# Optimization experiments

Hardware: AMD Instinct MI355X
Metric: run time of the kernel (lower is better)

Reference implementation:

```python
import jax
import jax.numpy as jnp
import numpy as np

NB_FEATURES = 512
DIM_EXPLOSION_FACTOR = 20
MB_DIM = NB_FEATURES * DIM_EXPLOSION_FACTOR  # 10240
NB_PROJ_ENTRIES = 6   # nonzeros per row of the random projection
HASH_LENGTH = 32      # k for k-winner-take-all
NB_CLASSES = 100
BATCH = 8192


def _make_rand_proj(key):
    # Sparse binary projection: each MB neuron samples NB_PROJ_ENTRIES inputs.
    r = jax.random.uniform(key, (MB_DIM, NB_FEATURES), dtype=jnp.float32)
    th = jax.lax.top_k(r, NB_PROJ_ENTRIES)[0][:, -1:]  # per-row k-th largest
    return (r >= th).astype(jnp.float32)  # [MB_DIM, NB_FEATURES], ~6 ones/row


def setup_inputs() -> dict:
    key = jax.random.key(0)
    k1, k2, k3, k4 = jax.random.split(key, 4)
    x = jax.random.normal(k1, (BATCH, NB_FEATURES), dtype=jnp.float32)
    w1 = _make_rand_proj(k2)
    # PositiveLinear params (kaiming-uniform-ish scale)
    bound = 1.0 / np.sqrt(MB_DIM)
    w2 = jax.random.uniform(k3, (NB_CLASSES, MB_DIM), dtype=jnp.float32,
                            minval=-bound, maxval=bound)
    b2 = jax.random.uniform(k4, (NB_CLASSES,), dtype=jnp.float32,
                            minval=-bound, maxval=bound)
    return {"x": x, "w1": w1, "w2": w2, "b2": b2}


def reference(x, w1, w2, b2):
    # MB projection: dense matmul with the (non-learned) random projection.
    h = jnp.einsum("bf,mf->bm", x, w1)  # [B, MB_DIM]
    # k-winner-take-all sparsify: keep the HASH_LENGTH largest values per row.
    th = jax.lax.top_k(h, HASH_LENGTH)[0][:, -1:]  # k-th largest per row
    h = jnp.where(h >= th, h, jnp.zeros((), h.dtype))
    # PositiveLinear: weights clamped to min=0 before the linear.
    w2c = jnp.maximum(w2, 0.0)
    return jnp.einsum("bm,cm->bc", h, w2c) + b2  # [B, NB_CLASSES]
```

## Files before the change

kernel.cpp:

```cpp
#include <hip/hip_runtime.h>
#include <stdint.h>

typedef unsigned int uint;
typedef unsigned short ushort;

#define NB_FEATURES 512
#define MB_DIM      10240
#define NB_CLASSES  100
#define BATCH       8192
#define KSEL        32
#define NTHR        256
#define VPT         40
#define MAXOVF      512

static __device__ __forceinline__ uint f2key(float f) {
    uint u = __float_as_uint(f);
    return u ^ (0x80000000u | (uint)((int)u >> 31));
}
static __device__ __forceinline__ float key2f(uint k) {
    uint u = k ^ (0x80000000u | (uint)(((int)~k) >> 31));
    return __uint_as_float(u);
}

__global__ __launch_bounds__(256) void k_extract(const float* __restrict__ w1,
                                                 uint2* __restrict__ idx2,
                                                 uint* __restrict__ ovfc,
                                                 uint2* __restrict__ ovfe) {
    __shared__ ushort scr[4][8];
    const int gw   = (blockIdx.x * 256 + threadIdx.x) >> 6;
    const int lane = threadIdx.x & 63;
    const int wid  = (threadIdx.x >> 6) & 3;

    const float* row = w1 + (size_t)gw * NB_FEATURES;
    const float4 a = *(const float4*)(row + lane * 8);
    const float4 b = *(const float4*)(row + lane * 8 + 4);
    const float v[8] = {a.x, a.y, a.z, a.w, b.x, b.y, b.z, b.w};
    int cnt = 0;
#pragma unroll
    for (int j = 0; j < 8; ++j) cnt += (v[j] > 0.5f);
    int p = cnt;
#pragma unroll
    for (int off = 1; off < 64; off <<= 1) {
        int n = __shfl_up(p, off, 64);
        if (lane >= off) p += n;
    }
    const int total = __shfl(p, 63, 64);
    int slot = p - cnt;

    if (lane < 8) scr[wid][lane] = (ushort)NB_FEATURES;
    __syncthreads();
#pragma unroll
    for (int j = 0; j < 8; ++j) {
        if (v[j] > 0.5f) {
            if (slot < 8) scr[wid][slot] = (ushort)(lane * 8 + j);
            slot++;
        }
    }
    __syncthreads();
    if (lane == 0) {
        const uint c0 = scr[wid][0], c1 = scr[wid][1], c2 = scr[wid][2];
        const uint c3 = scr[wid][3], c4 = scr[wid][4], c5 = scr[wid][5];
        const uint c6 = scr[wid][6], c7 = scr[wid][7];
        uint2 q;
        q.x = c0 | (c1 << 10) | (c2 << 20);
        q.y = c3 | (c4 << 10) | (c5 << 20);
        idx2[gw] = q;
        if (total > 6) {
            const uint s = atomicAdd(ovfc, 1u);
            if (s < MAXOVF) {
                uint2 e; e.x = (uint)gw; e.y = c6 | (c7 << 10);
                ovfe[s] = e;
            }
        }
    }
}

__global__ __launch_bounds__(256) void k_w2t(const float* __restrict__ w2,
                                             float* __restrict__ w2t) {
    const int i = blockIdx.x * 256 + threadIdx.x;
    if (i >= NB_CLASSES * MB_DIM) return;
    const int c = i / MB_DIM;
    const int m = i - c * MB_DIM;
    w2t[(size_t)m * NB_CLASSES + c] = fmaxf(w2[i], 0.0f);
}

template <bool USE_W2T>
__global__ __launch_bounds__(NTHR) void k_main(
    const float* __restrict__ x, const uint2* __restrict__ idx2,
    const uint* __restrict__ ovfc, const uint2* __restrict__ ovfe,
    const float* __restrict__ w2t, const float* __restrict__ w2,
    const float* __restrict__ b2, float* __restrict__ out)
{
    __shared__ float xs4[513 * 4];
    __shared__ float cand[512];
    __shared__ uint  s_wsum[4];
    __shared__ float s_piv[4];
    __shared__ float s_thf;
    __shared__ uint  s_cnt1;
    __shared__ uint  s_pref;
    __shared__ int   s_k;
    __shared__ uint  list_m[64];
    __shared__ float list_v[64];

    const int tid  = threadIdx.x;
    const int lane = tid & 63;
    const int wid  = tid >> 6;
    const int brow = blockIdx.x;

    {
        const float v0 = x[(size_t)brow * NB_FEATURES + tid];
        const float v1 = x[(size_t)brow * NB_FEATURES + tid + 256];
        float4 f0; f0.x = v0; f0.y = v0; f0.z = v0; f0.w = v0;
        float4 f1; f1.x = v1; f1.y = v1; f1.z = v1; f1.w = v1;
        *(float4*)&xs4[tid << 2]         = f0;
        *(float4*)&xs4[(tid + 256) << 2] = f1;
        if (tid == 0) {
            float4 z; z.x = 0.0f; z.y = 0.0f; z.z = 0.0f; z.w = 0.0f;
            *(float4*)&xs4[512 << 2] = z;
        }
        if (tid < 64) { list_m[tid] = 0u; list_v[tid] = 0.0f; }
    }
    __syncthreads();

    const float* xb = xs4 + (tid & 3);

    float vals[VPT];
#pragma unroll
    for (int i = 0; i < VPT; ++i) {
        const int m = tid + (i << 8);
        const uint2 q = idx2[m];
        float s = xb[(q.x & 1023u) << 2];
        s += xb[((q.x >> 10) & 1023u) << 2];
        s += xb[((q.x >> 20) & 1023u) << 2];
        s += xb[(q.y & 1023u) << 2];
        s += xb[((q.y >> 10) & 1023u) << 2];
        s += xb[((q.y >> 20) & 1023u) << 2];
        vals[i] = s;
    }

    {
        uint novf = *ovfc;
        if (novf > MAXOVF) novf = MAXOVF;
        for (uint e = 0; e < novf; ++e) {
            const uint2 ent = ovfe[e];
            const float add = xb[(ent.y & 1023u) << 2]
                            + xb[((ent.y >> 10) & 1023u) << 2];
            const int em = (int)ent.x;
#pragma unroll
            for (int i = 0; i < VPT; ++i) {
                if (em == tid + (i << 8)) vals[i] += add;
            }
        }
    }

    {
        float v = vals[0];
#pragma unroll
        for (int i = 1; i < VPT; ++i) v = fmaxf(v, vals[i]);
#pragma unroll
        for (int k = 2; k <= 64; k <<= 1) {
#pragma unroll
            for (int j = k >> 1; j > 0; j >>= 1) {
                const float pr = __shfl_xor(v, j, 64);
                const bool lower = (lane & j) == 0;
                const bool asc   = (lane & k) == 0;
                const float mn = fminf(v, pr), mx = fmaxf(v, pr);
                v = (lower == asc) ? mx : mn;
            }
        }
        if (lane == 31) s_piv[wid] = v;
    }
    __syncthreads();
    float pivot = fmaxf(fmaxf(s_piv[0], s_piv[1]), fmaxf(s_piv[2], s_piv[3]));

    int myc = 0;
#pragma unroll
    for (int i = 0; i < VPT; ++i) myc += (vals[i] >= pivot) ? 1 : 0;
    int p = myc;
#pragma unroll
    for (int off = 1; off < 64; off <<= 1) {
        int n = __shfl_up(p, off, 64);
        if (lane >= off) p += n;
    }
    if (lane == 63) s_wsum[wid] = (uint)p;
    __syncthreads();
    int base = p - myc;
    for (int w = 0; w < wid; ++w) base += (int)s_wsum[w];
    const int ctot = (int)(s_wsum[0] + s_wsum[1] + s_wsum[2] + s_wsum[3]);
    {
        int slot = base;
#pragma unroll
        for (int i = 0; i < VPT; ++i) {
            if (vals[i] >= pivot) {
                if (slot < 512) cand[slot] = vals[i];
                slot++;
            }
        }
    }
    __syncthreads();

    if (ctot <= 512) {
        for (int pos = tid; pos < ctot; pos += NTHR) {
            const float u = cand[pos];
            int rank = 0;
            for (int j = 0; j < ctot; ++j) {
                const float vv = cand[j];
                rank += ((vv > u) || (vv == u && j < pos)) ? 1 : 0;
            }
            if (rank == KSEL - 1) s_thf = u;
        }
    } else {
        if (tid == 0) { s_pref = 0u; s_k = KSEL; }
        __syncthreads();
        for (int bit = 31; bit >= 0; --bit) {
            const uint bmask = 1u << bit;
            const uint dmask = (bit == 31) ? 0u : (0xFFFFFFFFu << (bit + 1));
            const uint pref = s_pref;
            int mc = 0;
#pragma unroll
            for (int i = 0; i < VPT; ++i) {
                const uint k = f2key(vals[i]);
                mc += (((k & dmask) == pref) && (k & bmask)) ? 1 : 0;
            }
            if (tid == 0) s_cnt1 = 0;
            __syncthreads();
            if (mc) atomicAdd(&s_cnt1, (uint)mc);
            __syncthreads();
            if (tid == 0) {
                if ((int)s_cnt1 >= s_k) s_pref = pref | bmask;
                else s_k -= (int)s_cnt1;
            }
            __syncthreads();
        }
        if (tid == 0) s_thf = key2f(s_pref);
    }
    __syncthreads();
    const float thf = s_thf;

    int kc = 0;
#pragma unroll
    for (int i = 0; i < VPT; ++i) kc += (vals[i] >= thf) ? 1 : 0;
    int p2 = kc;
#pragma unroll
    for (int off = 1; off < 64; off <<= 1) {
        int n = __shfl_up(p2, off, 64);
        if (lane >= off) p2 += n;
    }
    if (lane == 63) s_wsum[wid] = (uint)p2;
    __syncthreads();
    int kbase = p2 - kc;
    for (int w = 0; w < wid; ++w) kbase += (int)s_wsum[w];
    {
        int slot = kbase;
#pragma unroll
        for (int i = 0; i < VPT; ++i) {
            if (vals[i] >= thf) {
                if (slot < 64) {
                    list_m[slot] = (uint)(tid + (i << 8));
                    list_v[slot] = vals[i];
                }
                slot++;
            }
        }
    }
    __syncthreads();

    if (tid < NB_CLASSES) {
        float a0 = b2[tid], a1 = 0.0f;
#pragma unroll
        for (int j = 0; j < 64; j += 2) {
            const uint m0 = list_m[j], m1 = list_m[j + 1];
            float w0, w1;
            if (USE_W2T) {
                w0 = w2t[(size_t)m0 * NB_CLASSES + tid];
                w1 = w2t[(size_t)m1 * NB_CLASSES + tid];
            } else {
                w0 = fmaxf(w2[(size_t)tid * MB_DIM + m0], 0.0f);
                w1 = fmaxf(w2[(size_t)tid * MB_DIM + m1], 0.0f);
            }
            a0 = fmaf(list_v[j],     w0, a0);
            a1 = fmaf(list_v[j + 1], w1, a1);
        }
        out[(size_t)brow * NB_CLASSES + tid] = a0 + a1;
    }
}

extern "C" void kernel_launch(void* const* d_in, const int* in_sizes, int n_in,
                              void* d_out, int out_size, void* d_ws, size_t ws_size,
                              hipStream_t stream) {
    const float* x  = (const float*)d_in[0];
    const float* w1 = (const float*)d_in[1];
    const float* w2 = (const float*)d_in[2];
    const float* b2 = (const float*)d_in[3];
    float* out = (float*)d_out;

    uint2* idx2 = (uint2*)d_ws;
    uint*  ovfc = (uint*)((char*)d_ws + 81920);
    uint2* ovfe = (uint2*)((char*)d_ws + 81928);
    const size_t W2T_OFF = 131072;
    float* w2t = (float*)((char*)d_ws + W2T_OFF);
    const bool use_w2t =
        ws_size >= W2T_OFF + (size_t)MB_DIM * NB_CLASSES * sizeof(float);

    hipMemsetAsync(ovfc, 0, sizeof(uint), stream);
    k_extract<<<(MB_DIM * 64) / 256, 256, 0, stream>>>(w1, idx2, ovfc, ovfe);
    if (use_w2t) {
        k_w2t<<<(MB_DIM * NB_CLASSES + 255) / 256, 256, 0, stream>>>(w2, w2t);
        k_main<true><<<BATCH, NTHR, 0, stream>>>(x, idx2, ovfc, ovfe, w2t, w2, b2, out);
    } else {
        k_main<false><<<BATCH, NTHR, 0, stream>>>(x, idx2, ovfc, ovfe, nullptr, w2, b2, out);
    }
}
```

Baseline: 193.7 us.

## Pack projection indices as byte offsets in uint4, drop overflow list and 4x x replication

The index table now stores eight 16-bit pre-scaled byte offsets per MB neuron in a uint4, with a pad sentinel, in place of six 10-bit indices plus a global overflow list. This removes the memset, the atomic overflow path and the per-block scan over overflow entries. The x row in LDS is no longer replicated four times, and index decoding becomes cheaper. It also adds a partial-unroll loop and an occupancy hint in launch_bounds, at the cost of 16-byte index loads and a branch for the seventh and eighth entries.

```diff
diff --git a/kernel.cpp b/kernel.cpp
--- a/kernel.cpp
+++ b/kernel.cpp
@@ -11,7 +11,8 @@
 #define KSEL        32
 #define NTHR        256
 #define VPT         40
-#define MAXOVF      512
+#define PADOFF      2048u
+#define PADPAIR     0x08000800u
 
 static __device__ __forceinline__ uint f2key(float f) {
     uint u = __float_as_uint(f);
@@ -23,9 +24,7 @@
 }
 
 __global__ __launch_bounds__(256) void k_extract(const float* __restrict__ w1,
-                                                 uint2* __restrict__ idx2,
-                                                 uint* __restrict__ ovfc,
-                                                 uint2* __restrict__ ovfe) {
+                                                 uint4* __restrict__ idx4) {
     __shared__ ushort scr[4][8];
     const int gw   = (blockIdx.x * 256 + threadIdx.x) >> 6;
     const int lane = threadIdx.x & 63;
@@ -44,34 +43,25 @@
         int n = __shfl_up(p, off, 64);
         if (lane >= off) p += n;
     }
-    const int total = __shfl(p, 63, 64);
     int slot = p - cnt;
 
-    if (lane < 8) scr[wid][lane] = (ushort)NB_FEATURES;
+    if (lane < 8) scr[wid][lane] = (ushort)PADOFF;
     __syncthreads();
 #pragma unroll
     for (int j = 0; j < 8; ++j) {
         if (v[j] > 0.5f) {
-            if (slot < 8) scr[wid][slot] = (ushort)(lane * 8 + j);
+            if (slot < 8) scr[wid][slot] = (ushort)((lane * 8 + j) * 4);
             slot++;
         }
     }
     __syncthreads();
     if (lane == 0) {
-        const uint c0 = scr[wid][0], c1 = scr[wid][1], c2 = scr[wid][2];
-        const uint c3 = scr[wid][3], c4 = scr[wid][4], c5 = scr[wid][5];
-        const uint c6 = scr[wid][6], c7 = scr[wid][7];
-        uint2 q;
-        q.x = c0 | (c1 << 10) | (c2 << 20);
-        q.y = c3 | (c4 << 10) | (c5 << 20);
-        idx2[gw] = q;
-        if (total > 6) {
-            const uint s = atomicAdd(ovfc, 1u);
-            if (s < MAXOVF) {
-                uint2 e; e.x = (uint)gw; e.y = c6 | (c7 << 10);
-                ovfe[s] = e;
-            }
-        }
+        uint4 q;
+        q.x = (uint)scr[wid][0] | ((uint)scr[wid][1] << 16);
+        q.y = (uint)scr[wid][2] | ((uint)scr[wid][3] << 16);
+        q.z = (uint)scr[wid][4] | ((uint)scr[wid][5] << 16);
+        q.w = (uint)scr[wid][6] | ((uint)scr[wid][7] << 16);
+        idx4[gw] = q;
     }
 }
 
@@ -84,14 +74,15 @@
     w2t[(size_t)m * NB_CLASSES + c] = fmaxf(w2[i], 0.0f);
 }
 
+#define LD(o) (*(const float*)((const char*)xs + (o)))
+
 template <bool USE_W2T>
-__global__ __launch_bounds__(NTHR) void k_main(
-    const float* __restrict__ x, const uint2* __restrict__ idx2,
-    const uint* __restrict__ ovfc, const uint2* __restrict__ ovfe,
+__global__ __launch_bounds__(NTHR, 8) void k_main(
+    const float* __restrict__ x, const uint4* __restrict__ idx4,
     const float* __restrict__ w2t, const float* __restrict__ w2,
     const float* __restrict__ b2, float* __restrict__ out)
 {
-    __shared__ float xs4[513 * 4];
+    __shared__ float xs[513];
     __shared__ float cand[512];
     __shared__ uint  s_wsum[4];
     __shared__ float s_piv[4];
@@ -108,48 +99,29 @@
     const int brow = blockIdx.x;
 
     {
-        const float v0 = x[(size_t)brow * NB_FEATURES + tid];
-        const float v1 = x[(size_t)brow * NB_FEATURES + tid + 256];
-        float4 f0; f0.x = v0; f0.y = v0; f0.z = v0; f0.w = v0;
-        float4 f1; f1.x = v1; f1.y = v1; f1.z = v1; f1.w = v1;
-        *(float4*)&xs4[tid << 2]         = f0;
-        *(float4*)&xs4[(tid + 256) << 2] = f1;
-        if (tid == 0) {
-            float4 z; z.x = 0.0f; z.y = 0.0f; z.z = 0.0f; z.w = 0.0f;
-            *(float4*)&xs4[512 << 2] = z;
-        }
+        xs[tid]       = x[(size_t)brow * NB_FEATURES + tid];
+        xs[tid + 256] = x[(size_t)brow * NB_FEATURES + tid + 256];
+        if (tid == 0) xs[512] = 0.0f;
         if (tid < 64) { list_m[tid] = 0u; list_v[tid] = 0.0f; }
     }
     __syncthreads();
 
-    const float* xb = xs4 + (tid & 3);
-
     float vals[VPT];
-#pragma unroll
-    for (int i = 0; i < VPT; ++i) {
-        const int m = tid + (i << 8);
-        const uint2 q = idx2[m];
-        float s = xb[(q.x & 1023u) << 2];
-        s += xb[((q.x >> 10) & 1023u) << 2];
-        s += xb[((q.x >> 20) & 1023u) << 2];
-        s += xb[(q.y & 1023u) << 2];
-        s += xb[((q.y >> 10) & 1023u) << 2];
-        s += xb[((q.y >> 20) & 1023u) << 2];
-        vals[i] = s;
-    }
-
-    {
-        uint novf = *ovfc;
-        if (novf > MAXOVF) novf = MAXOVF;
-        for (uint e = 0; e < novf; ++e) {
-            const uint2 ent = ovfe[e];
-            const float add = xb[(ent.y & 1023u) << 2]
-                            + xb[((ent.y >> 10) & 1023u) << 2];
-            const int em = (int)ent.x;
-#pragma unroll
-            for (int i = 0; i < VPT; ++i) {
-                if (em == tid + (i << 8)) vals[i] += add;
-            }
+    const uint4* ip = idx4 + tid;
+#pragma unroll 1
+    for (int ii = 0; ii < VPT / 2; ++ii) {
+#pragma unroll
+        for (int j = 0; j < 2; ++j) {
+            const int i = ii * 2 + j;
+            const uint4 q = ip[(size_t)i << 8];
+            const float s0 = LD(q.x & 0xFFFFu) + LD(q.x >> 16);
+            const float s1 = LD(q.y & 0xFFFFu) + LD(q.y >> 16);
+            const float s2 = LD(q.z & 0xFFFFu) + LD(q.z >> 16);
+            float s = (s0 + s1) + s2;
+            if (q.w != PADPAIR) {
+                s += LD(q.w & 0xFFFFu) + LD(q.w >> 16);
+            }
+            vals[i] = s;
         }
     }
 
@@ -171,7 +143,7 @@
         if (lane == 31) s_piv[wid] = v;
     }
     __syncthreads();
-    float pivot = fmaxf(fmaxf(s_piv[0], s_piv[1]), fmaxf(s_piv[2], s_piv[3]));
+    const float pivot = fmaxf(fmaxf(s_piv[0], s_piv[1]), fmaxf(s_piv[2], s_piv[3]));
 
     int myc = 0;
 #pragma unroll
@@ -294,20 +266,17 @@
     const float* b2 = (const float*)d_in[3];
     float* out = (float*)d_out;
 
-    uint2* idx2 = (uint2*)d_ws;
-    uint*  ovfc = (uint*)((char*)d_ws + 81920);
-    uint2* ovfe = (uint2*)((char*)d_ws + 81928);
-    const size_t W2T_OFF = 131072;
+    uint4* idx4 = (uint4*)d_ws;
+    const size_t W2T_OFF = 163840;
     float* w2t = (float*)((char*)d_ws + W2T_OFF);
     const bool use_w2t =
         ws_size >= W2T_OFF + (size_t)MB_DIM * NB_CLASSES * sizeof(float);
 
-    hipMemsetAsync(ovfc, 0, sizeof(uint), stream);
-    k_extract<<<(MB_DIM * 64) / 256, 256, 0, stream>>>(w1, idx2, ovfc, ovfe);
+    k_extract<<<(MB_DIM * 64) / 256, 256, 0, stream>>>(w1, idx4);
     if (use_w2t) {
         k_w2t<<<(MB_DIM * NB_CLASSES + 255) / 256, 256, 0, stream>>>(w2, w2t);
-        k_main<true><<<BATCH, NTHR, 0, stream>>>(x, idx2, ovfc, ovfe, w2t, w2, b2, out);
+        k_main<true><<<BATCH, NTHR, 0, stream>>>(x, idx4, w2t, w2, b2, out);
     } else {
-        k_main<false><<<BATCH, NTHR, 0, stream>>>(x, idx2, ovfc, ovfe, nullptr, w2, b2, out);
-    }
-}
+        k_main<false><<<BATCH, NTHR, 0, stream>>>(x, idx4, nullptr, w2, b2, out);
+    }
+}
```

Result: slower. 333.8 us (+72.3%).
